# Kernel tuning notes

Hardware: AMD Instinct MI355X
Metric: run time of the kernel (lower is better)

The kernel has to match this reference:

```python
import jax, jax.numpy as jnp
import numpy as np

N, F, H, ATTR = 128, 128, 8, 3
HU, HUE = [16, 8], [4, 2]


def setup_inputs() -> dict:
    key = jax.random.key(0)
    ks = iter(jax.random.split(key, 40))
    def g(shape):
        return jax.random.normal(next(ks), shape, dtype=jnp.float32) * 0.1
    M = N * N
    return dict(
        X=g((N, F)), A=g((ATTR, N, N)), E=g((ATTR, N, N)), e2n_adj=g((N, M)),
        Wn0=g((ATTR, H, F, HU[0])), bn0=jnp.zeros((ATTR, H, HU[0]), jnp.float32),
        an0_s=g((ATTR, H, HU[0])), an0_n=g((ATTR, H, HU[0])),
        Wn1=g((ATTR, H, H * HU[0], HU[1])), bn1=jnp.zeros((ATTR, H, HU[1]), jnp.float32),
        an1_s=g((ATTR, H, HU[1])), an1_n=g((ATTR, H, HU[1])),
        We0=g((H, ATTR, HUE[0])), be0=jnp.zeros((H, HUE[0]), jnp.float32),
        We1=g((H, H * HUE[0], HUE[1])), be1=jnp.zeros((H, HUE[1]), jnp.float32),
        Wct0=g((H, HU[0] + HUE[0], HU[0])), bct0=jnp.zeros((H, HU[0]), jnp.float32),
        Wct1=g((H, HU[1] + HUE[1], HU[1])), bct1=jnp.zeros((H, HU[1]), jnp.float32),
        ae0_s=g((H, HU[0])), ae0_n=g((H, HUE[0])),
        ae1_s=g((H, HU[1])), ae1_n=g((H, HUE[1])),
    )


def _leaky(x):
    return jnp.where(x >= 0, x, 0.2 * x)  # LeakyReLU(0.2)


def reference(X, A, E, e2n_adj,
              Wn0, bn0, an0_s, an0_n, Wn1, bn1, an1_s, an1_n,
              We0, be0, We1, be1, Wct0, bct0, Wct1, bct1,
              ae0_s, ae0_n, ae1_s, ae1_n):
    # Eval mode (dropout = identity). Heads are vectorized (leading h axis).
    nb_attr, n = E.shape[0], X.shape[0]
    E_e2n = E.reshape(nb_attr, -1).T  # [M, nb_attr], row-major flatten matches torch .view(-1,1)
    edge_layers = [(We0, be0, Wct0, bct0, ae0_s, ae0_n),
                   (We1, be1, Wct1, bct1, ae1_s, ae1_n)]
    attrs_out = []
    for attr in range(nb_attr):
        node_layers = [(Wn0[attr], bn0[attr], an0_s[attr], an0_n[attr]),
                       (Wn1[attr], bn1[attr], an1_s[attr], an1_n[attr])]
        X_head, X_edge, E_info = X, E_e2n, E[attr]
        h_list = [X]
        for (Wn, bn, an_s, an_n), (We, be, Wct, bct, ae_s, ae_n) in zip(node_layers, edge_layers):
            feat = jnp.einsum('nf,hfk->hnk', X_head, Wn)          # node features per head
            feat_e = jnp.einsum('mf,hfk->hmk', X_edge, We)        # edge features per head
            a_self = jnp.einsum('hnk,hk->hn', feat, ae_s)
            a_edge = jnp.einsum('hmk,hk->hm', feat_e, ae_n)
            # edge-to-node attention over all M = N*N edges
            alpha_e = jax.nn.softmax(_leaky(a_self[:, :, None] + a_edge[:, None, :]) + e2n_adj[None], axis=-1)
            nf_e = jnp.einsum('hnm,hmk->hnk', alpha_e, feat_e) + be[:, None, :]
            feat2 = jnp.einsum('hnc,hck->hnk', jnp.concatenate([feat, nf_e], axis=-1), Wct) + bct[:, None, :]
            s2 = jnp.einsum('hnk,hk->hn', feat2, an_s)
            n2 = jnp.einsum('hnk,hk->hn', feat2, an_n)
            dense = jnp.einsum('hij,jm->him', s2[:, :, None] + n2[:, None, :], E_info)  # [h,N,N]
            alpha = jax.nn.softmax(_leaky(dense) + A[attr][None], axis=-1)
            nf = jax.nn.elu(jnp.einsum('hnm,hmk->hnk', alpha, feat2) + bn[:, None, :])
            h1 = jnp.transpose(nf, (1, 0, 2)).reshape(n, -1)      # concat heads on feature axis
            h_list.append(h1)
            X_head = h1
            X_edge = jnp.transpose(feat_e, (1, 0, 2)).reshape(feat_e.shape[1], -1)
            E_info = alpha[-1]                                    # last head's attention matrix
        attrs_out.append(jnp.concatenate(h_list, axis=-1)[:, None, :])
    return jnp.concatenate(attrs_out, axis=1)                     # [N, nb_attr, F + 8*16 + 8*8]
```

## Files before the change

### kernel.cpp

```cpp
#include <hip/hip_runtime.h>

static constexpr int N = 128;
static constexpr int F = 128;
static constexpr int H = 8;
static constexpr int NATTR = 3;
static constexpr int M = N * N;
static constexpr int OUTW = 320;
static constexpr int MSL = 64;
static constexpr int CH = M / MSL;
static constexpr float LOG2E = 1.4426950408889634f;

__device__ __forceinline__ float leaky(float x) { return fmaxf(x, 0.2f * x); }
__device__ __forceinline__ int swz(int m) { return m ^ ((m >> 3) & 7); }

template <bool L1>
__global__ void __launch_bounds__(256)
k_ea(const float* __restrict__ E,
     const float* __restrict__ xsrc,
     int xStride,
     const float* __restrict__ Wn,
     const float* __restrict__ aes,
     const float* __restrict__ We0,
     const float* __restrict__ aen,
     const float* __restrict__ We1,
     const float* __restrict__ adj,
     float* __restrict__ part) {
    constexpr int KW = L1 ? 8 : 16;
    __shared__ __align__(16) float sV[4 * CH];
    __shared__ __align__(16) float sEx[CH * 4];
    __shared__ __align__(16) float sWv[12 * 128];
    __shared__ float sVa[12];
    __shared__ float sWc[24];

    int b = blockIdx.x;
    int ms = b & (MSL - 1);
    int nt = (b >> 6) & 7;
    int h0 = (b >> 9) * 4;
    int tid = threadIdx.x;
    int r = tid >> 4, l = tid & 15;
    int n = nt * 16 + r;
    int m0 = ms * CH;

    for (int idx = tid; idx < 12 * 128; idx += 256) {
        int c = idx >> 7, f = idx & 127;
        int a = c >> 2, h = h0 + (c & 3);
        const float* wp = Wn + ((size_t)(a * H + h) * F + f) * KW;
        const float* ap = aes + h * KW;
        float acc = 0.f;
#pragma unroll
        for (int k = 0; k < KW; ++k) acc += wp[k] * ap[k];
        sWv[idx] = acc * LOG2E;
    }
    if (L1) {
        if (tid < 24) {
            int hh = tid / 6, rem = tid % 6, at = rem >> 1, k2 = rem & 1;
            int h = h0 + hh;
            float acc = 0.f;
            for (int c = 0; c < 32; ++c)
                acc += We0[((c >> 2) * 3 + at) * 4 + (c & 3)] *
                       We1[(h * 32 + c) * 2 + k2];
            sWc[(hh * 3 + at) * 2 + k2] = acc;
        }
        __syncthreads();
    }
    if (tid < 12) {
        int hh = tid >> 2 == 0 ? tid / 3 : tid / 3;
        int at = tid % 3;
        hh = tid / 3;
        int h = h0 + hh;
        float acc = 0.f;
        if (!L1) {
#pragma unroll
            for (int k = 0; k < 4; ++k)
                acc += We0[(h * 3 + at) * 4 + k] * aen[h * 4 + k];
        } else {
#pragma unroll
            for (int k2 = 0; k2 < 2; ++k2)
                acc += sWc[(hh * 3 + at) * 2 + k2] * aen[h * 2 + k2];
        }
        sVa[hh * 3 + at] = acc * LOG2E;
    }
    __syncthreads();

    for (int mm = tid; mm < CH; mm += 256) {
        int m = m0 + mm;
        float e0 = E[m], e1 = E[M + m], e2 = E[2 * M + m];
        int mw = swz(mm);
        sEx[mw * 4 + 0] = e0;
        sEx[mw * 4 + 1] = e1;
        sEx[mw * 4 + 2] = e2;
        sEx[mw * 4 + 3] = 0.f;
#pragma unroll
        for (int hh = 0; hh < 4; ++hh)
            sV[hh * CH + mm] = sVa[hh * 3 + 0] * e0 + sVa[hh * 3 + 1] * e1 +
                               sVa[hh * 3 + 2] * e2;
    }
    __syncthreads();

    float u[NATTR][4];
#pragma unroll
    for (int a = 0; a < NATTR; ++a) {
        const float* xr = xsrc + (size_t)a * xStride + (size_t)n * F;
        float xv[8];
#pragma unroll
        for (int j = 0; j < 8; ++j) xv[j] = xr[l + 16 * j];
#pragma unroll
        for (int hh = 0; hh < 4; ++hh) {
            const float* wr = sWv + (a * 4 + hh) * 128;
            float d = 0.f;
#pragma unroll
            for (int j = 0; j < 8; ++j) d += xv[j] * wr[l + 16 * j];
#pragma unroll
            for (int off = 1; off < 16; off <<= 1) d += __shfl_xor(d, off);
            u[a][hh] = d;
        }
    }

    float sm[4][NATTR], q0[4][NATTR], q1[4][NATTR], q2[4][NATTR];
#pragma unroll
    for (int hh = 0; hh < 4; ++hh)
#pragma unroll
        for (int a = 0; a < NATTR; ++a) {
            sm[hh][a] = 0.f;
            q0[hh][a] = 0.f; q1[hh][a] = 0.f; q2[hh][a] = 0.f;
        }

    const float* adjp = adj + (size_t)n * M + m0;
    for (int i = l * 4; i < CH; i += 64) {
        const float4 av = *(const float4*)(adjp + i);
        float4 ev[4];
#pragma unroll
        for (int hh = 0; hh < 4; ++hh)
            ev[hh] = *(const float4*)&sV[hh * CH + i];
#pragma unroll
        for (int j = 0; j < 4; ++j) {
            float adjv = (&av.x)[j] * LOG2E;
            const float4 ex = *(const float4*)&sEx[swz(i + j) * 4];
#pragma unroll
            for (int hh = 0; hh < 4; ++hh) {
                float vv = (&ev[hh].x)[j];
#pragma unroll
                for (int a = 0; a < NATTR; ++a) {
                    float t = u[a][hh] + vv;
                    float p = __builtin_amdgcn_exp2f(fmaxf(t, 0.2f * t) + adjv);
                    sm[hh][a] += p;
                    q0[hh][a] += p * ex.x;
                    q1[hh][a] += p * ex.y;
                    q2[hh][a] += p * ex.z;
                }
            }
        }
    }

#pragma unroll
    for (int off = 1; off < 16; off <<= 1) {
#pragma unroll
        for (int hh = 0; hh < 4; ++hh)
#pragma unroll
            for (int a = 0; a < NATTR; ++a) {
                sm[hh][a] += __shfl_xor(sm[hh][a], off);
                q0[hh][a] += __shfl_xor(q0[hh][a], off);
                q1[hh][a] += __shfl_xor(q1[hh][a], off);
                q2[hh][a] += __shfl_xor(q2[hh][a], off);
            }
    }
    if (l == 0) {
#pragma unroll
        for (int hh = 0; hh < 4; ++hh)
#pragma unroll
            for (int a = 0; a < NATTR; ++a) {
                float* pp = part + (((size_t)ms * NATTR + a) * N + n) * 32 +
                            (h0 + hh) * 4;
                *(float4*)pp = make_float4(q0[hh][a], q1[hh][a], q2[hh][a],
                                           sm[hh][a]);
            }
    }
}

template <int K, int KE, bool FIRST>
__global__ void __launch_bounds__(256)
k_mid(const float* __restrict__ xsrc,
      int xStride,
      const float* __restrict__ Wn,
      const float* __restrict__ part,
      const float* __restrict__ We0,
      const float* __restrict__ We1,
      const float* __restrict__ be,
      const float* __restrict__ Wct,
      const float* __restrict__ bct,
      const float* __restrict__ ans,
      const float* __restrict__ ann,
      const float* __restrict__ X,
      float* __restrict__ out,
      float* __restrict__ feat2,
      float* __restrict__ s2,
      float* __restrict__ n2) {
    constexpr int CIN = K + KE;
    __shared__ __align__(16) float sWn[F * K];
    __shared__ __align__(16) float sW[CIN * K];
    __shared__ __align__(16) float sIn[32 * CIN];
    __shared__ __align__(16) float sF2[32 * K];

    int b = blockIdx.x;
    int nt = b & 3, h = (b >> 2) & 7, a = b >> 5;
    int n0 = nt * 32;
    int tid = threadIdx.x;

    for (int i = tid; i < F * K; i += 256)
        sWn[i] = Wn[(size_t)(a * H + h) * F * K + i];
    for (int i = tid; i < CIN * K; i += 256) sW[i] = Wct[h * CIN * K + i];

    {
        int r = tid >> 3, g = tid & 7;
        int n = n0 + r;
        float m0 = 0.f, m1 = 0.f, m2 = 0.f, sv = 0.f;
        for (int ms = g; ms < MSL; ms += 8) {
            const float4 v = *(const float4*)(
                part + (((size_t)ms * NATTR + a) * N + n) * 32 + h * 4);
            m0 += v.x; m1 += v.y; m2 += v.z; sv += v.w;
        }
#pragma unroll
        for (int off = 1; off < 8; off <<= 1) {
            m0 += __shfl_xor(m0, off);
            m1 += __shfl_xor(m1, off);
            m2 += __shfl_xor(m2, off);
            sv += __shfl_xor(sv, off);
        }
        if (g == 0) {
            float inv = 1.f / sv;
            float mom[3] = {m0, m1, m2};
            if (KE == 4) {
#pragma unroll
                for (int k = 0; k < 4; ++k) {
                    float acc = 0.f;
#pragma unroll
                    for (int at = 0; at < 3; ++at)
                        acc += We0[(h * 3 + at) * 4 + k] * mom[at];
                    sIn[r * CIN + K + k] = acc * inv + be[h * 4 + k];
                }
            } else {
                float wc[3][2];
#pragma unroll
                for (int at = 0; at < 3; ++at) {
                    float w0 = 0.f, w1 = 0.f;
                    for (int c = 0; c < 32; ++c) {
                        float we0 = We0[((c >> 2) * 3 + at) * 4 + (c & 3)];
                        w0 += we0 * We1[(h * 32 + c) * 2 + 0];
                        w1 += we0 * We1[(h * 32 + c) * 2 + 1];
                    }
                    wc[at][0] = w0; wc[at][1] = w1;
                }
#pragma unroll
                for (int k = 0; k < 2; ++k) {
                    float acc = wc[0][k] * mom[0] + wc[1][k] * mom[1] +
                                wc[2][k] * mom[2];
                    sIn[r * CIN + K + k] = acc * inv + be[h * 2 + k];
                }
            }
        }
    }
    if (FIRST && h == 0) {
        for (int i = tid; i < 32 * F; i += 256) {
            int n = n0 + (i >> 7);
            int f = i & (F - 1);
            out[(n * NATTR + a) * OUTW + f] = X[n * F + f];
        }
    }
    __syncthreads();

    for (int o = tid; o < 32 * K; o += 256) {
        int r = o / K, k = o % K;
        const float* xr = xsrc + (size_t)a * xStride + (size_t)(n0 + r) * F;
        float acc = 0.f;
        for (int f = 0; f < F; ++f) acc += xr[f] * sWn[f * K + k];
        sIn[r * CIN + k] = acc;
    }
    __syncthreads();

    for (int o = tid; o < 32 * K; o += 256) {
        int r = o / K, k = o % K;
        float acc = bct[h * K + k];
        for (int c = 0; c < CIN; ++c) acc += sIn[r * CIN + c] * sW[c * K + k];
        sF2[o] = acc;
        feat2[((size_t)(a * H + h) * N + n0 + r) * 16 + k] = acc;
    }
    __syncthreads();
    if (tid < 32) {
        int r = tid;
        float ss = 0.f, nn = 0.f;
        for (int k = 0; k < K; ++k) {
            ss += sF2[r * K + k] * ans[(a * H + h) * K + k];
            nn += sF2[r * K + k] * ann[(a * H + h) * K + k];
        }
        s2[(a * H + h) * N + n0 + r] = ss;
        n2[(a * H + h) * N + n0 + r] = nn;
    }
}

template <int K, bool FIRST>
__global__ void __launch_bounds__(256)
k_node(const float* __restrict__ feat2,
       const float* __restrict__ s2,
       const float* __restrict__ n2,
       const float* __restrict__ Einfo,
       const float* __restrict__ Amat,
       const float* __restrict__ bn,
       float* __restrict__ out, int outOff,
       float* __restrict__ xh_out,
       float* __restrict__ einfo_out) {
    __shared__ __align__(16) float sF2[N * K];
    __shared__ __align__(16) float sS2[N];
    __shared__ __align__(16) float sn2[N];
    __shared__ __align__(16) float sdE[N];
    __shared__ __align__(16) float scE[N];
    __shared__ __align__(16) float sAlpha[4 * N];
    __shared__ __align__(16) float sRed[256];

    int b = blockIdx.x;
    int itile = b & 7, h = (b >> 3) & 7, a = b >> 6;
    int tid = threadIdx.x;

    for (int i = tid; i < N * K; i += 256)
        sF2[i] = feat2[((size_t)(a * H + h) * N + i / K) * 16 + i % K];
    if (tid < N) {
        sS2[tid] = s2[(a * H + h) * N + tid];
        sn2[tid] = n2[(a * H + h) * N + tid];
    }
    __syncthreads();

    {
        int m = tid & 127, w = tid >> 7;
        const float* Ep = Einfo + (size_t)a * M;
        float dacc = 0.f, cacc = 0.f;
        for (int j = w * 64; j < w * 64 + 64; ++j) {
            float v = Ep[j * N + m];
            dacc += sn2[j] * v;
            cacc += v;
        }
        sRed[tid] = dacc;
        sAlpha[w * N + m] = cacc;
        __syncthreads();
        if (tid < N) {
            sdE[tid] = sRed[tid] + sRed[128 + tid];
            scE[tid] = sAlpha[tid] + sAlpha[N + tid];
        }
    }
    __syncthreads();

    for (int pass = 0; pass < 4; ++pass) {
        int r = tid >> 6;
        int lane = tid & 63;
        int i = itile * 16 + pass * 4 + r;
        float s = sS2[i];
        const float* Ap = Amat + ((size_t)a * N + i) * N;
        float v0 = leaky(s * scE[lane] + sdE[lane]) + Ap[lane];
        float v1 = leaky(s * scE[lane + 64] + sdE[lane + 64]) + Ap[lane + 64];
        float p0 = __expf(v0), p1 = __expf(v1);
        float ssum = p0 + p1;
#pragma unroll
        for (int off = 1; off < 64; off <<= 1) ssum += __shfl_xor(ssum, off);
        float inv = 1.f / ssum;
        float a0 = p0 * inv, a1 = p1 * inv;
        sAlpha[r * N + lane] = a0;
        sAlpha[r * N + lane + 64] = a1;
        if (FIRST && h == H - 1) {
            einfo_out[((size_t)a * N + i) * N + lane] = a0;
            einfo_out[((size_t)a * N + i) * N + lane + 64] = a1;
        }
        __syncthreads();
        {
            int rr = tid >> 6, g = (tid >> 4) & 3, k = tid & 15;
            float acc = 0.f;
            if (k < K) {
                for (int it = 0; it < 32; ++it) {
                    int mm = g + 4 * it;
                    acc += sAlpha[rr * N + mm] * sF2[mm * K + k];
                }
            }
            sRed[tid] = acc;
        }
        __syncthreads();
        {
            int rr = tid >> 6, k = tid & 63;
            if (k < K) {
                float tot = bn[(a * H + h) * K + k];
#pragma unroll
                for (int g = 0; g < 4; ++g) tot += sRed[rr * 64 + g * 16 + k];
                float e = tot > 0.f ? tot : __expf(tot) - 1.f;
                int i2 = itile * 16 + pass * 4 + rr;
                out[(i2 * NATTR + a) * OUTW + outOff + h * K + k] = e;
                if (FIRST)
                    xh_out[((size_t)a * N + i2) * F + h * K + k] = e;
            }
        }
        __syncthreads();
    }
}

extern "C" void kernel_launch(void* const* d_in, const int* in_sizes, int n_in,
                              void* d_out, int out_size, void* d_ws, size_t ws_size,
                              hipStream_t stream) {
    const float* X    = (const float*)d_in[0];
    const float* A    = (const float*)d_in[1];
    const float* E    = (const float*)d_in[2];
    const float* adj  = (const float*)d_in[3];
    const float* Wn0  = (const float*)d_in[4];
    const float* bn0  = (const float*)d_in[5];
    const float* an0s = (const float*)d_in[6];
    const float* an0n = (const float*)d_in[7];
    const float* Wn1  = (const float*)d_in[8];
    const float* bn1  = (const float*)d_in[9];
    const float* an1s = (const float*)d_in[10];
    const float* an1n = (const float*)d_in[11];
    const float* We0  = (const float*)d_in[12];
    const float* be0  = (const float*)d_in[13];
    const float* We1  = (const float*)d_in[14];
    const float* be1  = (const float*)d_in[15];
    const float* Wct0 = (const float*)d_in[16];
    const float* bct0 = (const float*)d_in[17];
    const float* Wct1 = (const float*)d_in[18];
    const float* bct1 = (const float*)d_in[19];
    const float* ae0s = (const float*)d_in[20];
    const float* ae0n = (const float*)d_in[21];
    const float* ae1s = (const float*)d_in[22];
    const float* ae1n = (const float*)d_in[23];
    float* out = (float*)d_out;

    float* p = (float*)d_ws;
    float* part  = p; p += (size_t)MSL * NATTR * N * 32;
    float* feat2 = p; p += NATTR * H * N * 16;
    float* s2b   = p; p += NATTR * H * N;
    float* n2b   = p; p += NATTR * H * N;
    float* einfo = p; p += NATTR * N * N;
    float* xh    = p; p += NATTR * N * F;

    k_ea<false><<<dim3(2 * 8 * MSL), dim3(256), 0, stream>>>(
        E, X, 0, Wn0, ae0s, We0, ae0n, nullptr, adj, part);
    k_mid<16, 4, true><<<dim3(96), dim3(256), 0, stream>>>(
        X, 0, Wn0, part, We0, nullptr, be0, Wct0, bct0, an0s, an0n, X, out,
        feat2, s2b, n2b);
    k_node<16, true><<<dim3(192), dim3(256), 0, stream>>>(
        feat2, s2b, n2b, E, A, bn0, out, F, xh, einfo);

    k_ea<true><<<dim3(2 * 8 * MSL), dim3(256), 0, stream>>>(
        E, xh, N * F, Wn1, ae1s, We0, ae1n, We1, adj, part);
    k_mid<8, 2, false><<<dim3(96), dim3(256), 0, stream>>>(
        xh, N * F, Wn1, part, We0, We1, be1, Wct1, bct1, an1s, an1n,
        nullptr, nullptr, feat2, s2b, n2b);
    k_node<8, false><<<dim3(192), dim3(256), 0, stream>>>(
        feat2, s2b, n2b, einfo, A, bn1, out, F + 128, nullptr, nullptr);
}
```

Before: 99.69 us.

## Precompute self-attention scores in a prep kernel and transpose partial-sum layout

```diff
diff --git a/kernel.cpp b/kernel.cpp
--- a/kernel.cpp
+++ b/kernel.cpp
@@ -13,22 +13,46 @@
 __device__ __forceinline__ float leaky(float x) { return fmaxf(x, 0.2f * x); }
 __device__ __forceinline__ int swz(int m) { return m ^ ((m >> 3) & 7); }
 
+template <int K>
+__global__ void __launch_bounds__(128)
+k_prep(const float* __restrict__ xsrc, int xStride,
+       const float* __restrict__ Wn,
+       const float* __restrict__ aes,
+       float* __restrict__ aself) {
+    int a = blockIdx.x / H, h = blockIdx.x % H;
+    __shared__ float wv[F];
+    int tid = threadIdx.x;
+    {
+        const float* wp = Wn + ((size_t)(a * H + h) * F + tid) * K;
+        const float* ap = aes + h * K;
+        float acc = 0.f;
+#pragma unroll
+        for (int k = 0; k < K; ++k) acc += wp[k] * ap[k];
+        wv[tid] = acc;
+    }
+    __syncthreads();
+    const float4* xr4 = (const float4*)(xsrc + (size_t)a * xStride + (size_t)tid * F);
+    float acc = 0.f;
+#pragma unroll 4
+    for (int f = 0; f < F / 4; ++f) {
+        float4 v = xr4[f];
+        acc += v.x * wv[f * 4 + 0] + v.y * wv[f * 4 + 1] +
+               v.z * wv[f * 4 + 2] + v.w * wv[f * 4 + 3];
+    }
+    aself[(a * H + h) * N + tid] = acc * LOG2E;
+}
+
 template <bool L1>
 __global__ void __launch_bounds__(256)
 k_ea(const float* __restrict__ E,
-     const float* __restrict__ xsrc,
-     int xStride,
-     const float* __restrict__ Wn,
-     const float* __restrict__ aes,
+     const float* __restrict__ aself,
      const float* __restrict__ We0,
      const float* __restrict__ aen,
      const float* __restrict__ We1,
      const float* __restrict__ adj,
      float* __restrict__ part) {
-    constexpr int KW = L1 ? 8 : 16;
     __shared__ __align__(16) float sV[4 * CH];
     __shared__ __align__(16) float sEx[CH * 4];
-    __shared__ __align__(16) float sWv[12 * 128];
     __shared__ float sVa[12];
     __shared__ float sWc[24];
 
@@ -41,16 +65,6 @@
     int n = nt * 16 + r;
     int m0 = ms * CH;
 
-    for (int idx = tid; idx < 12 * 128; idx += 256) {
-        int c = idx >> 7, f = idx & 127;
-        int a = c >> 2, h = h0 + (c & 3);
-        const float* wp = Wn + ((size_t)(a * H + h) * F + f) * KW;
-        const float* ap = aes + h * KW;
-        float acc = 0.f;
-#pragma unroll
-        for (int k = 0; k < KW; ++k) acc += wp[k] * ap[k];
-        sWv[idx] = acc * LOG2E;
-    }
     if (L1) {
         if (tid < 24) {
             int hh = tid / 6, rem = tid % 6, at = rem >> 1, k2 = rem & 1;
@@ -64,9 +78,7 @@
         __syncthreads();
     }
     if (tid < 12) {
-        int hh = tid >> 2 == 0 ? tid / 3 : tid / 3;
-        int at = tid % 3;
-        hh = tid / 3;
+        int hh = tid / 3, at = tid % 3;
         int h = h0 + hh;
         float acc = 0.f;
         if (!L1) {
@@ -95,26 +107,14 @@
             sV[hh * CH + mm] = sVa[hh * 3 + 0] * e0 + sVa[hh * 3 + 1] * e1 +
                                sVa[hh * 3 + 2] * e2;
     }
-    __syncthreads();
 
     float u[NATTR][4];
 #pragma unroll
-    for (int a = 0; a < NATTR; ++a) {
-        const float* xr = xsrc + (size_t)a * xStride + (size_t)n * F;
-        float xv[8];
-#pragma unroll
-        for (int j = 0; j < 8; ++j) xv[j] = xr[l + 16 * j];
-#pragma unroll
-        for (int hh = 0; hh < 4; ++hh) {
-            const float* wr = sWv + (a * 4 + hh) * 128;
-            float d = 0.f;
-#pragma unroll
-            for (int j = 0; j < 8; ++j) d += xv[j] * wr[l + 16 * j];
-#pragma unroll
-            for (int off = 1; off < 16; off <<= 1) d += __shfl_xor(d, off);
-            u[a][hh] = d;
-        }
-    }
+    for (int a = 0; a < NATTR; ++a)
+#pragma unroll
+        for (int hh = 0; hh < 4; ++hh)
+            u[a][hh] = aself[(a * H + h0 + hh) * N + n];
+    __syncthreads();
 
     float sm[4][NATTR], q0[4][NATTR], q1[4][NATTR], q2[4][NATTR];
 #pragma unroll
@@ -126,6 +126,7 @@
         }
 
     const float* adjp = adj + (size_t)n * M + m0;
+#pragma unroll 1
     for (int i = l * 4; i < CH; i += 64) {
         const float4 av = *(const float4*)(adjp + i);
         float4 ev[4];
@@ -169,8 +170,7 @@
         for (int hh = 0; hh < 4; ++hh)
 #pragma unroll
             for (int a = 0; a < NATTR; ++a) {
-                float* pp = part + (((size_t)ms * NATTR + a) * N + n) * 32 +
-                            (h0 + hh) * 4;
+                float* pp = part + ((((size_t)a * N + n) * H + h0 + hh) * MSL + ms) * 4;
                 *(float4*)pp = make_float4(q0[hh][a], q1[hh][a], q2[hh][a],
                                            sm[hh][a]);
             }
@@ -213,10 +213,10 @@
     {
         int r = tid >> 3, g = tid & 7;
         int n = n0 + r;
+        const float* pp = part + (((size_t)a * N + n) * H + h) * MSL * 4;
         float m0 = 0.f, m1 = 0.f, m2 = 0.f, sv = 0.f;
         for (int ms = g; ms < MSL; ms += 8) {
-            const float4 v = *(const float4*)(
-                part + (((size_t)ms * NATTR + a) * N + n) * 32 + h * 4);
+            const float4 v = *(const float4*)(pp + ms * 4);
             m0 += v.x; m1 += v.y; m2 += v.z; sv += v.w;
         }
 #pragma unroll
@@ -427,23 +427,26 @@
     float* out = (float*)d_out;
 
     float* p = (float*)d_ws;
-    float* part  = p; p += (size_t)MSL * NATTR * N * 32;
+    float* part  = p; p += (size_t)NATTR * N * H * MSL * 4;
+    float* aself = p; p += NATTR * H * N;
     float* feat2 = p; p += NATTR * H * N * 16;
     float* s2b   = p; p += NATTR * H * N;
     float* n2b   = p; p += NATTR * H * N;
     float* einfo = p; p += NATTR * N * N;
     float* xh    = p; p += NATTR * N * F;
 
+    k_prep<16><<<dim3(24), dim3(128), 0, stream>>>(X, 0, Wn0, ae0s, aself);
     k_ea<false><<<dim3(2 * 8 * MSL), dim3(256), 0, stream>>>(
-        E, X, 0, Wn0, ae0s, We0, ae0n, nullptr, adj, part);
+        E, aself, We0, ae0n, nullptr, adj, part);
     k_mid<16, 4, true><<<dim3(96), dim3(256), 0, stream>>>(
         X, 0, Wn0, part, We0, nullptr, be0, Wct0, bct0, an0s, an0n, X, out,
         feat2, s2b, n2b);
     k_node<16, true><<<dim3(192), dim3(256), 0, stream>>>(
         feat2, s2b, n2b, E, A, bn0, out, F, xh, einfo);
 
+    k_prep<8><<<dim3(24), dim3(128), 0, stream>>>(xh, N * F, Wn1, ae1s, aself);
     k_ea<true><<<dim3(2 * 8 * MSL), dim3(256), 0, stream>>>(
-        E, xh, N * F, Wn1, ae1s, We0, ae1n, We1, adj, part);
+        E, aself, We0, ae1n, We1, adj, part);
     k_mid<8, 2, false><<<dim3(96), dim3(256), 0, stream>>>(
         xh, N * F, Wn1, part, We0, We1, be1, Wct1, bct1, an1s, an1n,
         nullptr, nullptr, feat2, s2b, n2b);
```

Result: faster. 94.99 us (-4.7%).
